# Optimization experiments

Hardware: AMD Instinct MI355X
Metric: run time of the kernel (lower is better)

Reference implementation:

```python
import jax, jax.numpy as jnp
import numpy as np

HOPS = 2
BN_EPS = 1e-5


def _glorot(key, shape):
    fan_in = shape[-2]
    bound = 1.0 / np.sqrt(fan_in)
    return jax.random.uniform(key, shape, jnp.float32, -bound, bound)


def setup_inputs() -> dict:
    key = jax.random.key(0)
    ks = jax.random.split(key, 12)
    n, e = 50000, 800000
    in_c, hid, out_c = 128, 96, 64
    x = jax.random.normal(ks[0], (n, in_c), jnp.float32)
    edge_index = jax.random.randint(ks[1], (2, e), 0, n, jnp.int32)
    # MixHopLayer 0: hops+1 linears in_c -> hid (stacked)
    conv0_W = _glorot(ks[2], (HOPS + 1, in_c, hid))
    conv0_b = jnp.zeros((HOPS + 1, hid), jnp.float32)
    # MixHopLayer 1: hops+1 linears hid*(hops+1) -> out_c
    conv1_W = _glorot(ks[3], (HOPS + 1, hid * (HOPS + 1), out_c))
    conv1_b = jnp.zeros((HOPS + 1, out_c), jnp.float32)
    # BatchNorm1d(hid*(hops+1)) eval-mode params/buffers
    w = hid * (HOPS + 1)
    bn_gamma = jnp.ones((w,), jnp.float32)
    bn_beta = jnp.zeros((w,), jnp.float32)
    bn_mean = 0.1 * jax.random.normal(ks[4], (w,), jnp.float32)
    bn_var = jnp.ones((w,), jnp.float32) + 0.1 * jax.random.uniform(ks[5], (w,))
    # final projection out_c*(hops+1) -> out_c
    fp_W = _glorot(ks[6], (out_c * (HOPS + 1), out_c))
    fp_b = jnp.zeros((out_c,), jnp.float32)
    return dict(x=x, edge_index=edge_index, conv0_W=conv0_W, conv0_b=conv0_b,
                conv1_W=conv1_W, conv1_b=conv1_b, bn_gamma=bn_gamma, bn_beta=bn_beta,
                bn_mean=bn_mean, bn_var=bn_var, fp_W=fp_W, fp_b=fp_b)


def _gcn_norm(edge_index, n):
    # PyG gcn_norm with add_self_loops=True, improved=False, symmetric norm.
    row, col = edge_index[0], edge_index[1]
    loop = jnp.arange(n, dtype=edge_index.dtype)
    row = jnp.concatenate([row, loop])
    col = jnp.concatenate([col, loop])
    deg = jax.ops.segment_sum(jnp.ones_like(col, jnp.float32), col, num_segments=n)
    dinv = jnp.where(deg > 0, jax.lax.rsqrt(deg), 0.0)
    w = dinv[row] * dinv[col]
    return row, col, w


def _spmm_adj_t(row, col, w, x, n):
    # adj_t = SparseTensor(row=col, col=row, value=w): out[col] += w * x[row]
    return jax.ops.segment_sum(w[:, None] * x[row], col, num_segments=n)


def _mixhop_layer(x, W, b, row, col, w, n):
    xs = [x @ W[0] + b[0]]
    for j in range(1, HOPS + 1):
        xj = x @ W[j] + b[j]
        for _ in range(j):
            xj = _spmm_adj_t(row, col, w, xj, n)
        xs.append(xj)
    return jnp.concatenate(xs, axis=1)


def reference(x, edge_index, conv0_W, conv0_b, conv1_W, conv1_b,
              bn_gamma, bn_beta, bn_mean, bn_var, fp_W, fp_b):
    n = x.shape[0]
    row, col, w = _gcn_norm(edge_index, n)
    h = _mixhop_layer(x, conv0_W, conv0_b, row, col, w, n)
    # BatchNorm1d (eval) + ReLU; dropout is identity in eval
    h = bn_gamma * (h - bn_mean) * jax.lax.rsqrt(bn_var + BN_EPS) + bn_beta
    h = jax.nn.relu(h)
    h = _mixhop_layer(h, conv1_W, conv1_b, row, col, w, n)
    return h @ fp_W + fp_b
```

## Files before the change

kernel.cpp:

```cpp
#include <hip/hip_runtime.h>

#define IN_C 128
#define HID 96
#define OUT_C 64
#define W0C 288
#define W1C 192
#define CAP 5120
#define EPB 1024

typedef __bf16 bf16x8v __attribute__((ext_vector_type(8)));
typedef float  f32x4v  __attribute__((ext_vector_type(4)));


__global__ void k_combo_prep(const float* __restrict__ x, __bf16* __restrict__ xb, int n8,
                             const float* __restrict__ W0, const float* __restrict__ W1,
                             const float* __restrict__ Wf,
                             const float* __restrict__ gamma, const float* __restrict__ beta,
                             const float* __restrict__ mean, const float* __restrict__ var,
                             __bf16* __restrict__ w0t, __bf16* __restrict__ w1t,
                             __bf16* __restrict__ wft,
                             float* __restrict__ scale, float* __restrict__ shift,
                             int* __restrict__ zp, int nz,
                             int CB, int PB) {
    int b = blockIdx.x;
    if (b < CB) {
        int i = b * 256 + threadIdx.x;
        if (i >= n8) return;
        bf16x8v o;
#pragma unroll
        for (int q = 0; q < 8; q++) o[q] = (__bf16)x[i * 8 + q];
        *(bf16x8v*)(xb + (size_t)i * 8) = o;
    } else if (b < CB + PB) {
        const int T0 = 3 * IN_C * HID;
        const int T1 = 3 * W0C * OUT_C;
        const int T2 = W1C * OUT_C;
        int i = (b - CB) * 256 + threadIdx.x;
        if (i < T0) {
            int kn = IN_C * HID;
            int j = i / kn, r = i % kn;
            int k = r / HID, nn = r % HID;
            w0t[(size_t)j * kn + (size_t)nn * IN_C + k] = (__bf16)W0[i];
        } else if (i < T0 + T1) {
            int ii = i - T0;
            int kn = W0C * OUT_C;
            int j = ii / kn, r = ii % kn;
            int k = r / OUT_C, nn = r % OUT_C;
            w1t[(size_t)j * kn + (size_t)nn * W0C + k] = (__bf16)W1[ii];
        } else if (i < T0 + T1 + T2) {
            int ii = i - T0 - T1;
            int k = ii / OUT_C, nn = ii % OUT_C;
            wft[(size_t)nn * W1C + k] = (__bf16)Wf[ii];
        } else if (i < T0 + T1 + T2 + W0C) {
            int ii = i - T0 - T1 - T2;
            float s = gamma[ii] * rsqrtf(var[ii] + 1e-5f);
            scale[ii] = s;
            shift[ii] = beta[ii] - mean[ii] * s;
        }
    } else {
        int i = (b - CB - PB) * 256 + threadIdx.x;
        if (i < nz) zp[i] = 0;
    }
}

__global__ __launch_bounds__(256) void k_mega0(
        const int* __restrict__ row, const int* __restrict__ col,
        int* __restrict__ bcur ,
        int* __restrict__ binned, int e, int SB,
        const __bf16* __restrict__ xb, const __bf16* __restrict__ w0t ,
        const float* __restrict__ bias , __bf16* __restrict__ h,
        const float* __restrict__ scale, const float* __restrict__ shift, int M) {
    const int RS = 104;
    __shared__ __bf16 tile[128 * RS];
    int tid = threadIdx.x;
    if ((int)blockIdx.x < SB) {
        int* hist  = (int*)tile;
        int* basep = hist + 256;
        int e0 = blockIdx.x * EPB;
        int cnt = min(EPB, e - e0);
        hist[tid] = 0;
        __syncthreads();
        int rr[4], cc[4], rk[4];
#pragma unroll
        for (int k = 0; k < 4; k++) {
            int idx = tid + k * 256;
            if (idx < cnt) {
                rr[k] = row[e0 + idx];
                cc[k] = col[e0 + idx];
                rk[k] = atomicAdd(&hist[cc[k] >> 8], 1);
            }
        }
        __syncthreads();
        {
            int hv = hist[tid];
            if (hv > 0) basep[tid] = atomicAdd(&bcur[tid * 16], hv);
        }
        __syncthreads();
#pragma unroll
        for (int k = 0; k < 4; k++) {
            int idx = tid + k * 256;
            if (idx < cnt) {
                int b = cc[k] >> 8;
                int pos = basep[b] + rk[k];
                if (pos < CAP)
                    binned[(size_t)b * CAP + pos] = (rr[k] << 8) | (cc[k] & 255);
            }
        }
        return;
    }
    int wave = tid >> 6, lane = tid & 63;
    int ln = lane & 15, quad = lane >> 4;
    int rowBase = (blockIdx.x - SB) * 128;
    int waveRow = wave * 16;
    f32x4v acc[2][6];
#pragma unroll
    for (int u = 0; u < 2; u++)
#pragma unroll
        for (int t = 0; t < 6; t++) acc[u][t] = (f32x4v){0.f, 0.f, 0.f, 0.f};
    const __bf16* arow0 = xb + (size_t)(rowBase + waveRow + ln) * IN_C + quad * 8;
    const __bf16* arow1 = arow0 + (size_t)64 * IN_C;
#pragma unroll
    for (int k = 0; k < 4; k++) {
        bf16x8v a0 = *(const bf16x8v*)(arow0 + k * 32);
        bf16x8v a1 = *(const bf16x8v*)(arow1 + k * 32);
#pragma unroll
        for (int c = 0; c < 6; c++) {
            bf16x8v b = *(const bf16x8v*)(w0t + (size_t)(c * 16 + ln) * IN_C + k * 32 + quad * 8);
            acc[0][c] = __builtin_amdgcn_mfma_f32_16x16x32_bf16(a0, b, acc[0][c], 0, 0, 0);
            acc[1][c] = __builtin_amdgcn_mfma_f32_16x16x32_bf16(a1, b, acc[1][c], 0, 0, 0);
        }
    }
#pragma unroll
    for (int u = 0; u < 2; u++)
#pragma unroll
        for (int r = 0; r < 4; r++) {
            int lr = u * 64 + waveRow + quad * 4 + r;
#pragma unroll
            for (int c = 0; c < 6; c++) {
                int col2 = c * 16 + ln;
                float v = acc[u][c][r] + bias[col2];
                v = fmaxf(v * scale[col2] + shift[col2], 0.f);
                tile[lr * RS + col2] = (__bf16)v;
            }
        }
    __syncthreads();
#pragma unroll
    for (int s = 0; s < 6; s++) {
        int idx = tid + s * 256;
        int r = idx / 12, c8 = idx % 12;
        int grow = rowBase + r;
        if (grow < M)
            *(bf16x8v*)(h + (size_t)grow * W0C + c8 * 8) =
                *(const bf16x8v*)(tile + r * RS + c8 * 8);
    }
}

__global__ void k_deg_scan(const int* __restrict__ binned, const int* __restrict__ bcur,
                           int* __restrict__ counts, float* __restrict__ dinv,
                           int* __restrict__ bscan, int n, int nb) {
    __shared__ int s[256];
    int tid = threadIdx.x;
    if ((int)blockIdx.x == nb) {
        int v = (tid < nb) ? bcur[tid * 16] : 0;
        s[tid] = v;
        __syncthreads();
        for (int off = 1; off < 256; off <<= 1) {
            int t = (tid >= off) ? s[tid - off] : 0;
            __syncthreads();
            s[tid] += t;
            __syncthreads();
        }
        if (tid < nb) bscan[tid] = s[tid] - v;
        return;
    }
    s[tid] = 0;
    __syncthreads();
    int cnt = min(bcur[blockIdx.x * 16], CAP);
    const int* bin = binned + (size_t)blockIdx.x * CAP;
    for (int t = tid; t < cnt; t += 256)
        atomicAdd(&s[bin[t] & 255], 1);
    __syncthreads();
    int node = (blockIdx.x << 8) + tid;
    if (node < n) {
        int d = s[tid];
        counts[node] = d;
        dinv[node] = rsqrtf((float)(d + 1));
    }
}

__global__ __launch_bounds__(256) void k_bucket_sort(
        const int* __restrict__ binned, const int* __restrict__ counts,
        const int* __restrict__ bcur, const int* __restrict__ bscan,
        const float* __restrict__ dinv,
        int2* __restrict__ csr, int* __restrict__ row_ptr,
        float* __restrict__ arow, int n) {
    __shared__ int   s_pack[CAP];
    __shared__ int   s_ofs[256];
    __shared__ int   lcur[256];
    __shared__ float s_a[256];
    int tid = threadIdx.x;
    int node0 = blockIdx.x << 8;
    int base = bscan[blockIdx.x];
    int cnt  = min(bcur[blockIdx.x * 16], CAP);
    const int* bin = binned + (size_t)blockIdx.x * CAP;

    int node = node0 + tid;
    int cdeg = (node < n) ? counts[node] : 0;
    s_ofs[tid] = cdeg;
    __syncthreads();
    for (int o = 1; o < 256; o <<= 1) {
        int u = (tid >= o) ? s_ofs[tid - o] : 0;
        __syncthreads();
        s_ofs[tid] += u;
        __syncthreads();
    }
    int nodeOfs = s_ofs[tid] - cdeg;
    if (node < n) {
        row_ptr[node] = base + nodeOfs;
        if (node == n - 1) row_ptr[n] = base + nodeOfs + cdeg;
    }
    lcur[tid] = 0;
    __syncthreads();
    for (int t = tid; t < cnt; t += 256)
        atomicAdd(&lcur[bin[t] >> 16], 1);
    __syncthreads();
    {
        int v = lcur[tid];
        s_ofs[tid] = v;
        __syncthreads();
        for (int o = 1; o < 256; o <<= 1) {
            int u = (tid >= o) ? s_ofs[tid - o] : 0;
            __syncthreads();
            s_ofs[tid] += u;
            __syncthreads();
        }
        lcur[tid] = s_ofs[tid] - v;
    }
    __syncthreads();
    for (int t = tid; t < cnt; t += 256) {
        int p = bin[t];
        int pos = atomicAdd(&lcur[p >> 16], 1);
        s_pack[pos] = p;
    }
    __syncthreads();
    s_ofs[tid] = nodeOfs;
    lcur[tid] = 0;
    s_a[tid] = 0.f;
    __syncthreads();
    for (int t = tid; t < cnt; t += 256) {
        int p = s_pack[t];
        int r = p >> 8;
        int local = p & 255;
        int pos = s_ofs[local] + atomicAdd(&lcur[local], 1);
        float wv = dinv[r] * dinv[node0 + local];
        csr[base + pos] = make_int2(r, __float_as_int(wv));
        atomicAdd(&s_a[local], wv);
    }
    __syncthreads();
    if (node < n) {
        float d = dinv[node];
        arow[node] = s_a[tid] + d * d;
    }
}


__global__ __launch_bounds__(256) void k_mf_l0b(
        const __bf16* __restrict__ s1, const __bf16* __restrict__ w0t,
        const float* __restrict__ bias , const float* __restrict__ arow,
        __bf16* __restrict__ h, __bf16* __restrict__ tp,
        const float* __restrict__ scale, const float* __restrict__ shift, int M) {
    const int RS = 104;
    __shared__ __bf16 tile[64 * RS];
    int tid = threadIdx.x;
    int wave = tid >> 6, lane = tid & 63;
    int ln = lane & 15, quad = lane >> 4;
    int rowBase = blockIdx.x * 64;
    int waveRow = wave * 16;
    const __bf16* w1p = w0t + (size_t)1 * HID * IN_C;
    const __bf16* w2p = w0t + (size_t)2 * HID * IN_C;
    f32x4v acc[2][6];
#pragma unroll
    for (int j = 0; j < 2; j++)
#pragma unroll
        for (int t = 0; t < 6; t++) acc[j][t] = (f32x4v){0.f, 0.f, 0.f, 0.f};
    const __bf16* arow0 = s1 + (size_t)(rowBase + waveRow + ln) * IN_C + quad * 8;
#pragma unroll
    for (int k = 0; k < 4; k++) {
        bf16x8v a0 = *(const bf16x8v*)(arow0 + k * 32);
#pragma unroll
        for (int c = 0; c < 6; c++) {
            bf16x8v b1 = *(const bf16x8v*)(w1p + (size_t)(c * 16 + ln) * IN_C + k * 32 + quad * 8);
            bf16x8v b2 = *(const bf16x8v*)(w2p + (size_t)(c * 16 + ln) * IN_C + k * 32 + quad * 8);
            acc[0][c] = __builtin_amdgcn_mfma_f32_16x16x32_bf16(a0, b1, acc[0][c], 0, 0, 0);
            acc[1][c] = __builtin_amdgcn_mfma_f32_16x16x32_bf16(a0, b2, acc[1][c], 0, 0, 0);
        }
    }
    float avs[4];
#pragma unroll
    for (int r = 0; r < 4; r++)
        avs[r] = arow[rowBase + waveRow + quad * 4 + r];
#pragma unroll
    for (int jj = 0; jj < 2; jj++) {
        const float* bj = bias + (jj + 1) * HID;
#pragma unroll
        for (int r = 0; r < 4; r++) {
            int lr = waveRow + quad * 4 + r;
            float av = avs[r];
#pragma unroll
            for (int c = 0; c < 6; c++) {
                int col = c * 16 + ln;
                float v = acc[jj][c][r] + av * bj[col];
                if (jj == 0) v = fmaxf(v * scale[HID + col] + shift[HID + col], 0.f);
                tile[lr * RS + col] = (__bf16)v;
            }
        }
        __syncthreads();
#pragma unroll
        for (int s = 0; s < 3; s++) {
            int idx = tid + s * 256;
            int r = idx / 12, c8 = idx % 12;
            int grow = rowBase + r;
            if (grow < M) {
                __bf16* dst = (jj == 0) ? (h + (size_t)grow * W0C + HID)
                                        : (tp + (size_t)grow * HID);
                *(bf16x8v*)(dst + c8 * 8) = *(const bf16x8v*)(tile + r * RS + c8 * 8);
            }
        }
        __syncthreads();
    }
}

__global__ __launch_bounds__(256) void k_mf_l1m(
        const __bf16* __restrict__ hb, const __bf16* __restrict__ w1t ,
        const float* __restrict__ bias ,
        __bf16* __restrict__ g, __bf16* __restrict__ u12, int M) {
    const int RS = 72;
    __shared__ __bf16 tile[64 * RS];
    int tid = threadIdx.x;
    int wave = tid >> 6, lane = tid & 63;
    int ln = lane & 15, quad = lane >> 4;
    int rowBase = blockIdx.x * 64;
    int waveRow = wave * 16;
    f32x4v acc[3][4];
#pragma unroll
    for (int j = 0; j < 3; j++)
#pragma unroll
        for (int t = 0; t < 4; t++) acc[j][t] = (f32x4v){0.f, 0.f, 0.f, 0.f};
    const __bf16* arow0 = hb + (size_t)(rowBase + waveRow + ln) * W0C + quad * 8;
#pragma unroll
    for (int k = 0; k < 9; k++) {
        bf16x8v a0 = *(const bf16x8v*)(arow0 + k * 32);
#pragma unroll
        for (int c = 0; c < 4; c++) {
#pragma unroll
            for (int j = 0; j < 3; j++) {
                bf16x8v b = *(const bf16x8v*)(w1t + (size_t)j * OUT_C * W0C +
                                              (size_t)(c * 16 + ln) * W0C + k * 32 + quad * 8);
                acc[j][c] = __builtin_amdgcn_mfma_f32_16x16x32_bf16(a0, b, acc[j][c], 0, 0, 0);
            }
        }
    }
#pragma unroll
    for (int j = 0; j < 3; j++) {
        const float* bj = bias + j * OUT_C;
#pragma unroll
        for (int r = 0; r < 4; r++) {
            int lr = waveRow + quad * 4 + r;
#pragma unroll
            for (int c = 0; c < 4; c++) {
                int col = c * 16 + ln;
                tile[lr * RS + col] = (__bf16)(acc[j][c][r] + bj[col]);
            }
        }
        __syncthreads();
        __bf16* dst = (j == 0) ? g : u12;
        int ld = (j == 0) ? W1C : 128;
        int c0 = (j == 2) ? OUT_C : 0;
#pragma unroll
        for (int s = 0; s < 2; s++) {
            int idx = tid + s * 256;
            int r = idx / 8, c8 = idx % 8;
            int grow = rowBase + r;
            if (grow < M)
                *(bf16x8v*)(dst + (size_t)grow * ld + c0 + c8 * 8) =
                    *(const bf16x8v*)(tile + r * RS + c8 * 8);
        }
        __syncthreads();
    }
}

__global__ __launch_bounds__(256) void k_mf_fin(
        const __bf16* __restrict__ gb, const __bf16* __restrict__ wft ,
        const float* __restrict__ bias, float* __restrict__ out, int M) {
    const int RS = 68;
    __shared__ float tile[128 * RS];
    int tid = threadIdx.x;
    int wave = tid >> 6, lane = tid & 63;
    int ln = lane & 15, quad = lane >> 4;
    int rowBase = blockIdx.x * 128;
    int waveRow = wave * 16;
    f32x4v acc[2][4];
#pragma unroll
    for (int u = 0; u < 2; u++)
#pragma unroll
        for (int t = 0; t < 4; t++) acc[u][t] = (f32x4v){0.f, 0.f, 0.f, 0.f};
    const __bf16* arow0 = gb + (size_t)(rowBase + waveRow + ln) * W1C + quad * 8;
    const __bf16* arow1 = arow0 + (size_t)64 * W1C;
#pragma unroll
    for (int k = 0; k < 6; k++) {
        bf16x8v a0 = *(const bf16x8v*)(arow0 + k * 32);
        bf16x8v a1 = *(const bf16x8v*)(arow1 + k * 32);
#pragma unroll
        for (int c = 0; c < 4; c++) {
            bf16x8v b = *(const bf16x8v*)(wft + (size_t)(c * 16 + ln) * W1C + k * 32 + quad * 8);
            acc[0][c] = __builtin_amdgcn_mfma_f32_16x16x32_bf16(a0, b, acc[0][c], 0, 0, 0);
            acc[1][c] = __builtin_amdgcn_mfma_f32_16x16x32_bf16(a1, b, acc[1][c], 0, 0, 0);
        }
    }
#pragma unroll
    for (int u = 0; u < 2; u++)
#pragma unroll
        for (int r = 0; r < 4; r++) {
            int lr = u * 64 + waveRow + quad * 4 + r;
#pragma unroll
            for (int c = 0; c < 4; c++) {
                int col = c * 16 + ln;
                tile[lr * RS + col] = acc[u][c][r] + bias[col];
            }
        }
    __syncthreads();
#pragma unroll
    for (int s = 0; s < 8; s++) {
        int idx = tid + s * 256;
        int r = idx / 16, c4 = idx % 16;
        int grow = rowBase + r;
        if (grow < M)
            *(float4*)(out + (size_t)grow * OUT_C + c4 * 4) =
                *(const float4*)(tile + r * RS + c4 * 4);
    }
}

template <int C8, int NPB, bool BNRELU>
__global__ void k_spmm(const __bf16* __restrict__ xin, int ldx,
                       __bf16* __restrict__ xout, int ldo,
                       const int* __restrict__ row_ptr,
                       const int2* __restrict__ csr,
                       const float* __restrict__ dinv, int n,
                       const float* __restrict__ scale, const float* __restrict__ shift,
                       int chan0) {
    int c8 = threadIdx.x % C8;
    int nl = threadIdx.x / C8;
    int node = blockIdx.x * NPB + nl;
    if (node >= n) return;
    float di = dinv[node];
    float lw = di * di;
    float acc[8];
    {
        bf16x8v v = *(const bf16x8v*)(xin + (size_t)node * ldx + c8 * 8);
#pragma unroll
        for (int q = 0; q < 8; q++) acc[q] = lw * (float)v[q];
    }
    int start = row_ptr[node];
    int cnt = row_ptr[node + 1] - start;
    int k = 0;
    for (; k + 4 <= cnt; k += 4) {
        int2 p0 = csr[start + k + 0], p1 = csr[start + k + 1];
        int2 p2 = csr[start + k + 2], p3 = csr[start + k + 3];
        float w0 = __int_as_float(p0.y), w1 = __int_as_float(p1.y);
        float w2 = __int_as_float(p2.y), w3 = __int_as_float(p3.y);
        bf16x8v v0 = *(const bf16x8v*)(xin + (size_t)p0.x * ldx + c8 * 8);
        bf16x8v v1 = *(const bf16x8v*)(xin + (size_t)p1.x * ldx + c8 * 8);
        bf16x8v v2 = *(const bf16x8v*)(xin + (size_t)p2.x * ldx + c8 * 8);
        bf16x8v v3 = *(const bf16x8v*)(xin + (size_t)p3.x * ldx + c8 * 8);
#pragma unroll
        for (int q = 0; q < 8; q++)
            acc[q] += w0 * (float)v0[q] + w1 * (float)v1[q] +
                      w2 * (float)v2[q] + w3 * (float)v3[q];
    }
    for (; k < cnt; k++) {
        int2 p = csr[start + k];
        float w = __int_as_float(p.y);
        bf16x8v xv = *(const bf16x8v*)(xin + (size_t)p.x * ldx + c8 * 8);
#pragma unroll
        for (int q = 0; q < 8; q++) acc[q] += w * (float)xv[q];
    }
    bf16x8v o;
#pragma unroll
    for (int q = 0; q < 8; q++) {
        float v = acc[q];
        if (BNRELU) {
            int ch = chan0 + c8 * 8 + q;
            v = fmaxf(v * scale[ch] + shift[ch], 0.f);
        }
        o[q] = (__bf16)v;
    }
    *(bf16x8v*)(xout + (size_t)node * ldo + c8 * 8) = o;
}

template <int C8, int SPLIT, int NPB, bool BNA, bool BNB>
__global__ void k_spmm2(const __bf16* __restrict__ xin, int ldx,
                        __bf16* __restrict__ dstA, int ldA, int chanA,
                        __bf16* __restrict__ dstB, int ldB, int chanB,
                        const int* __restrict__ row_ptr,
                        const int2* __restrict__ csr,
                        const float* __restrict__ dinv, int n,
                        const float* __restrict__ scale, const float* __restrict__ shift) {
    int c8 = threadIdx.x % C8;
    int nl = threadIdx.x / C8;
    int node = blockIdx.x * NPB + nl;
    if (node >= n) return;
    float di = dinv[node];
    float lw = di * di;
    float acc[8];
    {
        bf16x8v v = *(const bf16x8v*)(xin + (size_t)node * ldx + c8 * 8);
#pragma unroll
        for (int q = 0; q < 8; q++) acc[q] = lw * (float)v[q];
    }
    int start = row_ptr[node];
    int cnt = row_ptr[node + 1] - start;
    int k = 0;
    for (; k + 4 <= cnt; k += 4) {
        int2 p0 = csr[start + k + 0], p1 = csr[start + k + 1];
        int2 p2 = csr[start + k + 2], p3 = csr[start + k + 3];
        float w0 = __int_as_float(p0.y), w1 = __int_as_float(p1.y);
        float w2 = __int_as_float(p2.y), w3 = __int_as_float(p3.y);
        bf16x8v v0 = *(const bf16x8v*)(xin + (size_t)p0.x * ldx + c8 * 8);
        bf16x8v v1 = *(const bf16x8v*)(xin + (size_t)p1.x * ldx + c8 * 8);
        bf16x8v v2 = *(const bf16x8v*)(xin + (size_t)p2.x * ldx + c8 * 8);
        bf16x8v v3 = *(const bf16x8v*)(xin + (size_t)p3.x * ldx + c8 * 8);
#pragma unroll
        for (int q = 0; q < 8; q++)
            acc[q] += w0 * (float)v0[q] + w1 * (float)v1[q] +
                      w2 * (float)v2[q] + w3 * (float)v3[q];
    }
    for (; k < cnt; k++) {
        int2 p = csr[start + k];
        float w = __int_as_float(p.y);
        bf16x8v xv = *(const bf16x8v*)(xin + (size_t)p.x * ldx + c8 * 8);
#pragma unroll
        for (int q = 0; q < 8; q++) acc[q] += w * (float)xv[q];
    }
    bool isA = c8 < SPLIT;
    __bf16* dst = isA ? dstA : dstB;
    int ld   = isA ? ldA : ldB;
    int lc8  = isA ? c8 : c8 - SPLIT;
    int chan = isA ? chanA : chanB;
    bool bn  = isA ? BNA : BNB;
    bf16x8v o;
#pragma unroll
    for (int q = 0; q < 8; q++) {
        float v = acc[q];
        if (bn) {
            int ch = chan + lc8 * 8 + q;
            v = fmaxf(v * scale[ch] + shift[ch], 0.f);
        }
        o[q] = (__bf16)v;
    }
    *(bf16x8v*)(dst + (size_t)node * ld + lc8 * 8) = o;
}


extern "C" void kernel_launch(void* const* d_in, const int* in_sizes, int n_in,
                              void* d_out, int out_size, void* d_ws, size_t ws_size,
                              hipStream_t stream) {
    const int n = in_sizes[0] / IN_C;
    const int e = in_sizes[1] / 2;

    const float* x    = (const float*)d_in[0];
    const int*   ei   = (const int*)d_in[1];
    const float* W0   = (const float*)d_in[2];
    const float* b0   = (const float*)d_in[3];
    const float* W1   = (const float*)d_in[4];
    const float* b1   = (const float*)d_in[5];
    const float* bn_g = (const float*)d_in[6];
    const float* bn_b = (const float*)d_in[7];
    const float* bn_m = (const float*)d_in[8];
    const float* bn_v = (const float*)d_in[9];
    const float* Wf   = (const float*)d_in[10];
    const float* bf   = (const float*)d_in[11];
    float* out = (float*)d_out;

    const int* e_row = ei;
    const int* e_col = ei + e;

    char* ws = (char*)d_ws;
    size_t off = 0;
    auto alloc = [&](size_t bytes) -> void* {
        void* p = ws + off;
        off += (bytes + 255) & ~(size_t)255;
        return p;
    };
    const int NP = n + 128;
    int nb = (n + 255) / 256;

    int*    counts  = (int*)alloc((size_t)(n + 256 * 16) * 4);
    int*    bcur    = counts + n;
    int*    row_ptr = (int*)alloc((size_t)(n + 1) * 4);
    int*    bscan   = (int*)alloc(256 * 4);
    float*  dinv    = (float*)alloc((size_t)n * 4);
    float*  arow    = (float*)alloc((size_t)NP * 4);
    int*    binned  = (int*)alloc((size_t)nb * CAP * 4);
    int2*   csr     = (int2*)alloc((size_t)e * 8);
    float*  bnscale = (float*)alloc(W0C * 4);
    float*  bnshift = (float*)alloc(W0C * 4);
    __bf16* xb  = (__bf16*)alloc((size_t)NP * IN_C * 2);
    __bf16* w0t = (__bf16*)alloc((size_t)3 * HID * IN_C * 2);
    __bf16* w1t = (__bf16*)alloc((size_t)3 * OUT_C * W0C * 2);
    __bf16* wft = (__bf16*)alloc((size_t)OUT_C * W1C * 2);
    __bf16* s1  = (__bf16*)alloc((size_t)NP * 128 * 2);
    __bf16* tp  = (__bf16*)alloc((size_t)NP * HID * 2);
    __bf16* h   = (__bf16*)alloc((size_t)NP * W0C * 2);
    __bf16* g   = (__bf16*)alloc((size_t)NP * W1C * 2);
    __bf16* u12 = s1;
    __bf16* up  = tp;

    int n8 = n * IN_C / 8;
    int nz = 256 * 16;
    int ptotal = 3 * IN_C * HID + 3 * W0C * OUT_C + W1C * OUT_C + W0C;
    int CB = (n8 + 255) / 256;
    int PB = (ptotal + 255) / 256;
    int ZB = (nz + 255) / 256;
    k_combo_prep<<<dim3(CB + PB + ZB), dim3(256), 0, stream>>>(
        x, xb, n8, W0, W1, Wf, bn_g, bn_b, bn_m, bn_v,
        w0t, w1t, wft, bnscale, bnshift, bcur, nz, CB, PB);

    int SB = (e + EPB - 1) / EPB;
    int GG = (n + 127) / 128;
    k_mega0<<<dim3(SB + GG), dim3(256), 0, stream>>>(
        e_row, e_col, bcur, binned, e, SB,
        xb, w0t, b0, h, bnscale, bnshift, n);

    k_deg_scan<<<dim3(nb + 1), dim3(256), 0, stream>>>(binned, bcur, counts, dinv,
                                                       bscan, n, nb);

    k_bucket_sort<<<dim3(nb), dim3(256), 0, stream>>>(binned, counts, bcur, bscan, dinv,
                                                      csr, row_ptr, arow, n);

    dim3 g64((n + 63) / 64);

    k_spmm<16, 16, false><<<dim3((n + 15) / 16), dim3(256), 0, stream>>>(
        xb, IN_C, s1, 128, row_ptr, csr, dinv, n, nullptr, nullptr, 0);
    k_mf_l0b<<<g64, dim3(256), 0, stream>>>(s1, w0t, b0, arow, h, tp, bnscale, bnshift, n);
    k_spmm<12, 16, true><<<dim3((n + 15) / 16), dim3(192), 0, stream>>>(
        tp, HID, h + 2 * HID, W0C, row_ptr, csr, dinv, n, bnscale, bnshift, 2 * HID);

    k_mf_l1m<<<g64, dim3(256), 0, stream>>>(h, w1t, b1, g, u12, n);

    k_spmm2<16, 8, 16, false, false><<<dim3((n + 15) / 16), dim3(256), 0, stream>>>(
        u12, 128, g + OUT_C, W1C, 0, up, OUT_C, 0,
        row_ptr, csr, dinv, n, nullptr, nullptr);
    k_spmm<8, 32, false><<<dim3((n + 31) / 32), dim3(256), 0, stream>>>(
        up, OUT_C, g + 2 * OUT_C, W1C, row_ptr, csr, dinv, n, nullptr, nullptr, 0);

    k_mf_fin<<<dim3((n + 127) / 128), dim3(256), 0, stream>>>(g, wft, bf, out, n);
}
```

Baseline: 318.9 us.

## Merge degree/scan/sort into one kernel and recompute edge weights in SpMM

Folds the degree count, the bucket prefix scan and the bucket sort into a single kernel: each block redundantly scans the bucket counts and computes its own degrees, which removes a launch and the counts/bscan buffers. The CSR now stores only source indices, so that array is half the size, and edge weights are recomputed as dinv[src]*dinv[dst] inside each SpMM. The arow row sums move into the first SpMM pass. This trades smaller CSR traffic and one fewer launch for an extra gather of dinv per edge in every SpMM, plus a redundant per-block scan.

Measured after the change: 316.4 us. About the same (-0.8%).

```diff
diff --git a/kernel.cpp b/kernel.cpp
--- a/kernel.cpp
+++ b/kernel.cpp
@@ -154,57 +154,37 @@
     }
 }
 
-__global__ void k_deg_scan(const int* __restrict__ binned, const int* __restrict__ bcur,
-                           int* __restrict__ counts, float* __restrict__ dinv,
-                           int* __restrict__ bscan, int n, int nb) {
-    __shared__ int s[256];
+__global__ __launch_bounds__(256) void k_bucket_all(
+        const int* __restrict__ binned, const int* __restrict__ bcur,
+        float* __restrict__ dinv, int* __restrict__ csrs, int* __restrict__ row_ptr,
+        int n, int nb) {
+    __shared__ int s_pack[CAP];
+    __shared__ int s_ofs[256];
+    __shared__ int lcur[256];
+    __shared__ int s_scan[256];
     int tid = threadIdx.x;
-    if ((int)blockIdx.x == nb) {
-        int v = (tid < nb) ? bcur[tid * 16] : 0;
-        s[tid] = v;
-        __syncthreads();
-        for (int off = 1; off < 256; off <<= 1) {
-            int t = (tid >= off) ? s[tid - off] : 0;
-            __syncthreads();
-            s[tid] += t;
-            __syncthreads();
-        }
-        if (tid < nb) bscan[tid] = s[tid] - v;
-        return;
-    }
-    s[tid] = 0;
-    __syncthreads();
-    int cnt = min(bcur[blockIdx.x * 16], CAP);
-    const int* bin = binned + (size_t)blockIdx.x * CAP;
+    int b = blockIdx.x;
+    int node0 = b << 8;
+    int v = (tid < nb) ? bcur[tid * 16] : 0;
+    s_scan[tid] = v;
+    __syncthreads();
+    for (int o = 1; o < 256; o <<= 1) {
+        int u = (tid >= o) ? s_scan[tid - o] : 0;
+        __syncthreads();
+        s_scan[tid] += u;
+        __syncthreads();
+    }
+    int base = (b > 0) ? s_scan[b - 1] : 0;
+    int cnt = min(bcur[b * 16], CAP);
+    const int* bin = binned + (size_t)b * CAP;
+    lcur[tid] = 0;
+    __syncthreads();
     for (int t = tid; t < cnt; t += 256)
-        atomicAdd(&s[bin[t] & 255], 1);
-    __syncthreads();
-    int node = (blockIdx.x << 8) + tid;
-    if (node < n) {
-        int d = s[tid];
-        counts[node] = d;
-        dinv[node] = rsqrtf((float)(d + 1));
-    }
-}
-
-__global__ __launch_bounds__(256) void k_bucket_sort(
-        const int* __restrict__ binned, const int* __restrict__ counts,
-        const int* __restrict__ bcur, const int* __restrict__ bscan,
-        const float* __restrict__ dinv,
-        int2* __restrict__ csr, int* __restrict__ row_ptr,
-        float* __restrict__ arow, int n) {
-    __shared__ int   s_pack[CAP];
-    __shared__ int   s_ofs[256];
-    __shared__ int   lcur[256];
-    __shared__ float s_a[256];
-    int tid = threadIdx.x;
-    int node0 = blockIdx.x << 8;
-    int base = bscan[blockIdx.x];
-    int cnt  = min(bcur[blockIdx.x * 16], CAP);
-    const int* bin = binned + (size_t)blockIdx.x * CAP;
-
+        atomicAdd(&lcur[bin[t] & 255], 1);
+    __syncthreads();
+    int cdeg = lcur[tid];
     int node = node0 + tid;
-    int cdeg = (node < n) ? counts[node] : 0;
+    if (node < n) dinv[node] = rsqrtf((float)(cdeg + 1));
     s_ofs[tid] = cdeg;
     __syncthreads();
     for (int o = 1; o < 256; o <<= 1) {
@@ -224,8 +204,8 @@
         atomicAdd(&lcur[bin[t] >> 16], 1);
     __syncthreads();
     {
-        int v = lcur[tid];
-        s_ofs[tid] = v;
+        int vv = lcur[tid];
+        s_ofs[tid] = vv;
         __syncthreads();
         for (int o = 1; o < 256; o <<= 1) {
             int u = (tid >= o) ? s_ofs[tid - o] : 0;
@@ -233,7 +213,7 @@
             s_ofs[tid] += u;
             __syncthreads();
         }
-        lcur[tid] = s_ofs[tid] - v;
+        lcur[tid] = s_ofs[tid] - vv;
     }
     __syncthreads();
     for (int t = tid; t < cnt; t += 256) {
@@ -244,21 +224,13 @@
     __syncthreads();
     s_ofs[tid] = nodeOfs;
     lcur[tid] = 0;
-    s_a[tid] = 0.f;
     __syncthreads();
     for (int t = tid; t < cnt; t += 256) {
         int p = s_pack[t];
         int r = p >> 8;
         int local = p & 255;
         int pos = s_ofs[local] + atomicAdd(&lcur[local], 1);
-        float wv = dinv[r] * dinv[node0 + local];
-        csr[base + pos] = make_int2(r, __float_as_int(wv));
-        atomicAdd(&s_a[local], wv);
-    }
-    __syncthreads();
-    if (node < n) {
-        float d = dinv[node];
-        arow[node] = s_a[tid] + d * d;
+        csrs[base + pos] = r;
     }
 }
 
@@ -439,14 +411,14 @@
     }
 }
 
-template <int C8, int NPB, bool BNRELU>
+template <int C8, int NPB, bool BNRELU, bool AROW>
 __global__ void k_spmm(const __bf16* __restrict__ xin, int ldx,
                        __bf16* __restrict__ xout, int ldo,
                        const int* __restrict__ row_ptr,
-                       const int2* __restrict__ csr,
+                       const int* __restrict__ csrs,
                        const float* __restrict__ dinv, int n,
                        const float* __restrict__ scale, const float* __restrict__ shift,
-                       int chan0) {
+                       int chan0, float* __restrict__ arow) {
     int c8 = threadIdx.x % C8;
     int nl = threadIdx.x / C8;
     int node = blockIdx.x * NPB + nl;
@@ -459,30 +431,34 @@
 #pragma unroll
         for (int q = 0; q < 8; q++) acc[q] = lw * (float)v[q];
     }
+    float aw = lw;
     int start = row_ptr[node];
     int cnt = row_ptr[node + 1] - start;
+    const int* cp = csrs + start;
     int k = 0;
     for (; k + 4 <= cnt; k += 4) {
-        int2 p0 = csr[start + k + 0], p1 = csr[start + k + 1];
-        int2 p2 = csr[start + k + 2], p3 = csr[start + k + 3];
-        float w0 = __int_as_float(p0.y), w1 = __int_as_float(p1.y);
-        float w2 = __int_as_float(p2.y), w3 = __int_as_float(p3.y);
-        bf16x8v v0 = *(const bf16x8v*)(xin + (size_t)p0.x * ldx + c8 * 8);
-        bf16x8v v1 = *(const bf16x8v*)(xin + (size_t)p1.x * ldx + c8 * 8);
-        bf16x8v v2 = *(const bf16x8v*)(xin + (size_t)p2.x * ldx + c8 * 8);
-        bf16x8v v3 = *(const bf16x8v*)(xin + (size_t)p3.x * ldx + c8 * 8);
+        int s0 = cp[k + 0], s1 = cp[k + 1], s2 = cp[k + 2], s3 = cp[k + 3];
+        float w0 = dinv[s0] * di, w1 = dinv[s1] * di;
+        float w2 = dinv[s2] * di, w3 = dinv[s3] * di;
+        bf16x8v v0 = *(const bf16x8v*)(xin + (size_t)s0 * ldx + c8 * 8);
+        bf16x8v v1 = *(const bf16x8v*)(xin + (size_t)s1 * ldx + c8 * 8);
+        bf16x8v v2 = *(const bf16x8v*)(xin + (size_t)s2 * ldx + c8 * 8);
+        bf16x8v v3 = *(const bf16x8v*)(xin + (size_t)s3 * ldx + c8 * 8);
 #pragma unroll
         for (int q = 0; q < 8; q++)
             acc[q] += w0 * (float)v0[q] + w1 * (float)v1[q] +
                       w2 * (float)v2[q] + w3 * (float)v3[q];
+        if (AROW) aw += w0 + w1 + w2 + w3;
     }
     for (; k < cnt; k++) {
-        int2 p = csr[start + k];
-        float w = __int_as_float(p.y);
-        bf16x8v xv = *(const bf16x8v*)(xin + (size_t)p.x * ldx + c8 * 8);
+        int s = cp[k];
+        float w = dinv[s] * di;
+        bf16x8v xv = *(const bf16x8v*)(xin + (size_t)s * ldx + c8 * 8);
 #pragma unroll
         for (int q = 0; q < 8; q++) acc[q] += w * (float)xv[q];
-    }
+        if (AROW) aw += w;
+    }
+    if (AROW && c8 == 0) arow[node] = aw;
     bf16x8v o;
 #pragma unroll
     for (int q = 0; q < 8; q++) {
@@ -501,7 +477,7 @@
                         __bf16* __restrict__ dstA, int ldA, int chanA,
                         __bf16* __restrict__ dstB, int ldB, int chanB,
                         const int* __restrict__ row_ptr,
-                        const int2* __restrict__ csr,
+                        const int* __restrict__ csrs,
                         const float* __restrict__ dinv, int n,
                         const float* __restrict__ scale, const float* __restrict__ shift) {
     int c8 = threadIdx.x % C8;
@@ -518,25 +494,25 @@
     }
     int start = row_ptr[node];
     int cnt = row_ptr[node + 1] - start;
+    const int* cp = csrs + start;
     int k = 0;
     for (; k + 4 <= cnt; k += 4) {
-        int2 p0 = csr[start + k + 0], p1 = csr[start + k + 1];
-        int2 p2 = csr[start + k + 2], p3 = csr[start + k + 3];
-        float w0 = __int_as_float(p0.y), w1 = __int_as_float(p1.y);
-        float w2 = __int_as_float(p2.y), w3 = __int_as_float(p3.y);
-        bf16x8v v0 = *(const bf16x8v*)(xin + (size_t)p0.x * ldx + c8 * 8);
-        bf16x8v v1 = *(const bf16x8v*)(xin + (size_t)p1.x * ldx + c8 * 8);
-        bf16x8v v2 = *(const bf16x8v*)(xin + (size_t)p2.x * ldx + c8 * 8);
-        bf16x8v v3 = *(const bf16x8v*)(xin + (size_t)p3.x * ldx + c8 * 8);
+        int s0 = cp[k + 0], s1 = cp[k + 1], s2 = cp[k + 2], s3 = cp[k + 3];
+        float w0 = dinv[s0] * di, w1 = dinv[s1] * di;
+        float w2 = dinv[s2] * di, w3 = dinv[s3] * di;
+        bf16x8v v0 = *(const bf16x8v*)(xin + (size_t)s0 * ldx + c8 * 8);
+        bf16x8v v1 = *(const bf16x8v*)(xin + (size_t)s1 * ldx + c8 * 8);
+        bf16x8v v2 = *(const bf16x8v*)(xin + (size_t)s2 * ldx + c8 * 8);
+        bf16x8v v3 = *(const bf16x8v*)(xin + (size_t)s3 * ldx + c8 * 8);
 #pragma unroll
         for (int q = 0; q < 8; q++)
             acc[q] += w0 * (float)v0[q] + w1 * (float)v1[q] +
                       w2 * (float)v2[q] + w3 * (float)v3[q];
     }
     for (; k < cnt; k++) {
-        int2 p = csr[start + k];
-        float w = __int_as_float(p.y);
-        bf16x8v xv = *(const bf16x8v*)(xin + (size_t)p.x * ldx + c8 * 8);
+        int s = cp[k];
+        float w = dinv[s] * di;
+        bf16x8v xv = *(const bf16x8v*)(xin + (size_t)s * ldx + c8 * 8);
 #pragma unroll
         for (int q = 0; q < 8; q++) acc[q] += w * (float)xv[q];
     }
@@ -593,14 +569,12 @@
     const int NP = n + 128;
     int nb = (n + 255) / 256;
 
-    int*    counts  = (int*)alloc((size_t)(n + 256 * 16) * 4);
-    int*    bcur    = counts + n;
+    int*    bcur    = (int*)alloc((size_t)256 * 16 * 4);
     int*    row_ptr = (int*)alloc((size_t)(n + 1) * 4);
-    int*    bscan   = (int*)alloc(256 * 4);
     float*  dinv    = (float*)alloc((size_t)n * 4);
     float*  arow    = (float*)alloc((size_t)NP * 4);
     int*    binned  = (int*)alloc((size_t)nb * CAP * 4);
-    int2*   csr     = (int2*)alloc((size_t)e * 8);
+    int*    csrs    = (int*)alloc((size_t)e * 4);
     float*  bnscale = (float*)alloc(W0C * 4);
     float*  bnshift = (float*)alloc(W0C * 4);
     __bf16* xb  = (__bf16*)alloc((size_t)NP * IN_C * 2);
@@ -630,27 +604,26 @@
         e_row, e_col, bcur, binned, e, SB,
         xb, w0t, b0, h, bnscale, bnshift, n);
 
-    k_deg_scan<<<dim3(nb + 1), dim3(256), 0, stream>>>(binned, bcur, counts, dinv,
-                                                       bscan, n, nb);
-
-    k_bucket_sort<<<dim3(nb), dim3(256), 0, stream>>>(binned, counts, bcur, bscan, dinv,
-                                                      csr, row_ptr, arow, n);
+    k_bucket_all<<<dim3(nb), dim3(256), 0, stream>>>(binned, bcur, dinv, csrs,
+                                                     row_ptr, n, nb);
 
     dim3 g64((n + 63) / 64);
 
-    k_spmm<16, 16, false><<<dim3((n + 15) / 16), dim3(256), 0, stream>>>(
-        xb, IN_C, s1, 128, row_ptr, csr, dinv, n, nullptr, nullptr, 0);
+    k_spmm<16, 16, false, true><<<dim3((n + 15) / 16), dim3(256), 0, stream>>>(
+        xb, IN_C, s1, 128, row_ptr, csrs, dinv, n, nullptr, nullptr, 0, arow);
     k_mf_l0b<<<g64, dim3(256), 0, stream>>>(s1, w0t, b0, arow, h, tp, bnscale, bnshift, n);
-    k_spmm<12, 16, true><<<dim3((n + 15) / 16), dim3(192), 0, stream>>>(
-        tp, HID, h + 2 * HID, W0C, row_ptr, csr, dinv, n, bnscale, bnshift, 2 * HID);
+    k_spmm<12, 16, true, false><<<dim3((n + 15) / 16), dim3(192), 0, stream>>>(
+        tp, HID, h + 2 * HID, W0C, row_ptr, csrs, dinv, n, bnscale, bnshift,
+        2 * HID, nullptr);
 
     k_mf_l1m<<<g64, dim3(256), 0, stream>>>(h, w1t, b1, g, u12, n);
 
     k_spmm2<16, 8, 16, false, false><<<dim3((n + 15) / 16), dim3(256), 0, stream>>>(
         u12, 128, g + OUT_C, W1C, 0, up, OUT_C, 0,
-        row_ptr, csr, dinv, n, nullptr, nullptr);
-    k_spmm<8, 32, false><<<dim3((n + 31) / 32), dim3(256), 0, stream>>>(
-        up, OUT_C, g + 2 * OUT_C, W1C, row_ptr, csr, dinv, n, nullptr, nullptr, 0);
+        row_ptr, csrs, dinv, n, nullptr, nullptr);
+    k_spmm<8, 32, false, false><<<dim3((n + 31) / 32), dim3(256), 0, stream>>>(
+        up, OUT_C, g + 2 * OUT_C, W1C, row_ptr, csrs, dinv, n, nullptr, nullptr,
+        0, nullptr);
 
     k_mf_fin<<<dim3((n + 127) / 128), dim3(256), 0, stream>>>(g, wft, bf, out, n);
 }
```
